# Kernel optimization log

Hardware: AMD Instinct MI355X
Metric: run time of the kernel (lower is better)

## Reference

```python
import jax, jax.numpy as jnp
import numpy as np
from jax import lax

KSIZE = 3
STRIDE = 1
RATE = 2
SCALE = 10.0
GROUPS = 4
RATES = (1, 2, 4, 8)
ESCAPE_NAN = 1e-4


def extract_patches(x, kernel, stride):
    # x: [N,C,H,W]; ZeroPad2d(1) when kernel != 1, then sliding windows.
    pad = 0 if kernel == 1 else 1
    x = jnp.pad(x, ((0, 0), (0, 0), (pad, pad), (pad, pad)))
    N, C, H, W = x.shape
    oh = (H - kernel) // stride + 1
    ow = (W - kernel) // stride + 1
    r = jnp.arange(oh)[:, None] * stride + jnp.arange(kernel)[None, :]  # [oh,k]
    c = jnp.arange(ow)[:, None] * stride + jnp.arange(kernel)[None, :]  # [ow,k]
    p = x[:, :, r[:, :, None, None], c[None, None, :, :]]  # [N,C,oh,k,ow,k]
    p = p.transpose(0, 2, 4, 1, 3, 5)  # [N,oh,ow,C,k,k] (matches torch unfold order)
    return p.reshape(N, oh * ow, C, kernel, kernel)


def make_mask_c(H, W):
    # Vectorized version of the O(H*W) nested python loop: 4-neighbor patch bias.
    ii, jj = jnp.meshgrid(jnp.arange(H), jnp.arange(W), indexing='ij')
    p = ii * W + jj
    mc = jnp.zeros((H * W, H, W), jnp.float32)
    mc = mc.at[p[:, 1:] - 1, ii[:, 1:], jj[:, 1:]].set(1.0)        # j>=1
    mc = mc.at[p[:, :-1] + 1, ii[:, :-1], jj[:, :-1]].set(1.0)     # j<=W-2
    mc = mc.at[p[:-1] + W, ii[:-1], jj[:-1]].set(1.0)              # i<=H-2
    mc = mc.at[p[1:] - W, ii[1:], jj[1:]].set(1.0)                 # i>=1
    return mc


def atn_conv(x1, x2, mask, mask_all, fuse_w, fuse_b):
    N, C1, H1, W1 = x1.shape
    _, C2, H2, W2 = x2.shape
    kernel = 2 * RATE
    # patch banks
    raw_w = extract_patches(x1, kernel, RATE * STRIDE)          # [N,L,C1,4,4]
    w = extract_patches(x2, KSIZE, STRIDE)                      # [N,L,C2,3,3]
    # mask interpolated to x2 size with align_corners=True == identity here
    m = extract_patches(mask, KSIZE, STRIDE)                    # [N,L,1,3,3]
    m = m.mean(axis=(2, 3, 4))                                  # [N,L]
    mm = (m == 0.0).astype(x2.dtype)                            # 1 = valid patch
    mask_c = make_mask_c(H2, W2)                                # [L,H2,W2]
    pad = 0 if KSIZE == 1 else 1
    kt = kernel - 1 - 1  # conv_transpose padding=1 -> equiv fwd pad k-1-p

    def per_batch(xi, wi, raw_wi, mi, ma):
        # xi [C2,H2,W2], wi [L,C2,3,3], raw_wi [L,C1,4,4], mi [L], ma [1,H2,W2]
        norm = jnp.sqrt(jnp.sum(wi * wi, axis=(1, 2, 3), keepdims=True))
        wi_n = wi / jnp.maximum(norm, ESCAPE_NAN)
        yi = lax.conv_general_dilated(xi[None], wi_n, (1, 1), [(pad, pad), (pad, pad)],
                                      dimension_numbers=('NCHW', 'OIHW', 'NCHW'))[0]  # [L,H2,W2]
        mi_b = mi[:, None, None]
        yi = yi * mi_b * ma
        yi = jax.nn.softmax(yi * SCALE, axis=0)
        yi = yi + yi * mask_c * 0.5
        yi = yi * mi_b * ma
        yi = jnp.maximum(yi, 1e-8)
        # conv_transpose2d(yi, raw_wi, stride=RATE, padding=1)
        w_t = jnp.flip(raw_wi, axis=(-2, -1))  # [L,C1,4,4] used as IOHW
        out = lax.conv_general_dilated(yi[None], w_t, (1, 1), [(kt, kt), (kt, kt)],
                                       lhs_dilation=(RATE, RATE),
                                       dimension_numbers=('NCHW', 'IOHW', 'NCHW'))[0]
        return out / 4.0  # [C1,H1,W1]

    y = jax.vmap(per_batch)(x2, w, raw_w, mm, mask_all)          # [N,C1,H1,W1]

    # fuse: 4 dilated conv+relu branches, concat on channels
    outs = []
    for g in range(GROUPS):
        d = RATES[g]
        o = lax.conv_general_dilated(y, fuse_w[g], (1, 1), [(d, d), (d, d)],
                                     rhs_dilation=(d, d),
                                     dimension_numbers=('NCHW', 'OIHW', 'NCHW'))
        outs.append(jax.nn.relu(o + fuse_b[g][None, :, None, None]))
    return jnp.concatenate(outs, axis=1)


def setup_inputs() -> dict:
    key = jax.random.key(0)
    k1, k2, k3, k4, k5 = jax.random.split(key, 5)
    N, C, H2, W2 = 2, 128, 48, 48
    x1 = jax.random.normal(k1, (N, C, 2 * H2, 2 * W2), jnp.float32)
    x2 = jax.random.normal(k2, (N, C, H2, W2), jnp.float32)
    mask = jnp.zeros((N, 1, H2, W2), jnp.float32).at[:, :, 12:36, 12:36].set(1.0)  # 1 = hole
    mask_all = jax.random.uniform(k3, (N, 1, H2, W2), jnp.float32)
    out_pg = 64 // GROUPS
    fuse_w = jax.random.normal(k4, (GROUPS, out_pg, C, 3, 3), jnp.float32) * 0.02
    fuse_b = jax.random.normal(k5, (GROUPS, out_pg), jnp.float32) * 0.02
    return {'x1': x1, 'x2': x2, 'mask': mask, 'mask_all': mask_all,
            'fuse_w': fuse_w, 'fuse_b': fuse_b}


def reference(x1, x2, mask, mask_all, fuse_w, fuse_b):
    return atn_conv(x1, x2, mask, mask_all, fuse_w, fuse_b)
```

## Files before the change

kernel.cpp:

```cpp
#include <hip/hip_runtime.h>
#include <math.h>

typedef unsigned short u16;
typedef unsigned int   u32;
typedef float f32x4 __attribute__((ext_vector_type(4)));
typedef short bfx8  __attribute__((ext_vector_type(8)));

#define NB   2
#define CCH  128
#define HS   48
#define LL   2304
#define KW   2048
#define HO   96
#define PIX  9216
#define VHALF ((size_t)LL * KW)

#define XTH_B 0
#define XTL_B 1179648
#define PXN_B 2359296
#define NRM_B 2377728
#define MM_B  2396160
#define WF_B  2414592
#define WT_B  2562048
#define S_B   11999232
#define TBD_B S_B
#define V_B   (S_B + 10616832)
#define Z_B   33232896
#define YT_B  54466560

__device__ __forceinline__ u16 f2bf(float f) {
    u32 u = __float_as_uint(f);
    u32 r = (u + 0x7fffu + ((u >> 16) & 1u)) >> 16;
    return (u16)r;
}
__device__ __forceinline__ float bf2f(u16 h) {
    return __uint_as_float(((u32)h) << 16);
}
__device__ __forceinline__ void gll16(const void* g, void* l) {
    __builtin_amdgcn_global_load_lds((const __attribute__((address_space(1))) void*)g,
                                     (__attribute__((address_space(3))) void*)l, 16, 0, 0);
}

__global__ __launch_bounds__(256) void xprep_k(const float* __restrict__ x2,
                                               u16* __restrict__ Xh, u16* __restrict__ Xl,
                                               float* __restrict__ pxn) {
    __shared__ float lt[32][130];
    int n = blockIdx.z;
    int pix0 = blockIdx.x * 32;
    int tid = threadIdx.x;
    #pragma unroll
    for (int i = tid; i < 32 * 128; i += 256) {
        int c = i >> 5, p = i & 31;
        lt[p][c] = x2[((size_t)(n * CCH + c)) * LL + pix0 + p];
    }
    __syncthreads();
    #pragma unroll
    for (int i = tid; i < 32 * 128; i += 256) {
        int p = i >> 7, c = i & 127;
        float v = lt[p][c];
        u16 h = f2bf(v);
        size_t o = (size_t)(n * LL + pix0 + p) * CCH + c;
        Xh[o] = h;
        Xl[o] = f2bf(v - bf2f(h));
    }
    if (tid < 32) {
        float s = 0.0f;
        for (int c = 0; c < CCH; c++) { float t = lt[tid][c]; s += t * t; }
        pxn[n * LL + pix0 + tid] = s;
    }
}

__global__ __launch_bounds__(256) void boxnorm_k(const float* __restrict__ pxn,
                                                 const float* __restrict__ mask,
                                                 float* __restrict__ rnorm,
                                                 float* __restrict__ mmb) {
    int n = blockIdx.z;
    int p = blockIdx.x * 256 + threadIdx.x;
    int i = p / HS, j = p - (p / HS) * HS;
    float s = 0.0f, msum = 0.0f;
    for (int di = -1; di <= 1; di++)
        for (int dj = -1; dj <= 1; dj++) {
            int ii = i + di, jj = j + dj;
            if (ii >= 0 && ii < HS && jj >= 0 && jj < HS) {
                s += pxn[n * LL + ii * HS + jj];
                msum += mask[(n * HS + ii) * HS + jj];
            }
        }
    rnorm[n * LL + p] = 1.0f / fmaxf(sqrtf(s), 1e-4f);
    mmb[n * LL + p] = (msum == 0.0f) ? 1.0f : 0.0f;
}

__global__ __launch_bounds__(256) void sgemm_k(const u16* __restrict__ Xh, const u16* __restrict__ Xl,
                                               float* __restrict__ S) {
    __shared__ __align__(16) u16 Ah[4096], Al[4096], Bh[4096], Bl[4096];
    int tid = threadIdx.x, w = tid >> 6, lane = tid & 63;
    int m0 = blockIdx.x * 128, n0 = blockIdx.y * 128;
    int srow = lane & 15, sk = (lane >> 4) * 8;
    size_t a1 = (size_t)(m0 + w * 16 + srow) * CCH + sk;
    size_t a2 = a1 + (size_t)64 * CCH;
    size_t b1 = (size_t)(n0 + w * 16 + srow) * CCH + sk;
    size_t b2 = b1 + (size_t)64 * CCH;
    int wm = (w >> 1) * 64, wn = (w & 1) * 64;
    int ga = (w >> 1) * 4, gb = (w & 1) * 4;
    f32x4 acc[4][4];
    #pragma unroll
    for (int i = 0; i < 4; i++)
        #pragma unroll
        for (int j = 0; j < 4; j++) acc[i][j] = (f32x4)0.0f;

    for (int k0 = 0; k0 < CCH; k0 += 32) {
        if (k0) __syncthreads();
        gll16(Xh + a1 + k0, Ah + w * 512);
        gll16(Xh + a2 + k0, Ah + (w + 4) * 512);
        gll16(Xl + a1 + k0, Al + w * 512);
        gll16(Xl + a2 + k0, Al + (w + 4) * 512);
        gll16(Xh + b1 + k0, Bh + w * 512);
        gll16(Xh + b2 + k0, Bh + (w + 4) * 512);
        gll16(Xl + b1 + k0, Bl + w * 512);
        gll16(Xl + b2 + k0, Bl + (w + 4) * 512);
        __syncthreads();
        bfx8 ah[4], al[4], bh[4], bl[4];
        #pragma unroll
        for (int i = 0; i < 4; i++) {
            ah[i] = *(const bfx8*)&Ah[(ga + i) * 512 + lane * 8];
            al[i] = *(const bfx8*)&Al[(ga + i) * 512 + lane * 8];
        }
        #pragma unroll
        for (int j = 0; j < 4; j++) {
            bh[j] = *(const bfx8*)&Bh[(gb + j) * 512 + lane * 8];
            bl[j] = *(const bfx8*)&Bl[(gb + j) * 512 + lane * 8];
        }
        #pragma unroll
        for (int i = 0; i < 4; i++)
            #pragma unroll
            for (int j = 0; j < 4; j++) {
                acc[i][j] = __builtin_amdgcn_mfma_f32_16x16x32_bf16(ah[i], bh[j], acc[i][j], 0, 0, 0);
                acc[i][j] = __builtin_amdgcn_mfma_f32_16x16x32_bf16(ah[i], bl[j], acc[i][j], 0, 0, 0);
                acc[i][j] = __builtin_amdgcn_mfma_f32_16x16x32_bf16(al[i], bh[j], acc[i][j], 0, 0, 0);
            }
    }
    #pragma unroll
    for (int j = 0; j < 4; j++) {
        int col = n0 + wn + j * 16 + (lane & 15);
        #pragma unroll
        for (int i = 0; i < 4; i++) {
            int rbase = m0 + wm + i * 16 + (lane >> 4) * 4;
            #pragma unroll
            for (int r = 0; r < 4; r++)
                S[(size_t)(rbase + r) * LL + col] = acc[i][j][r];
        }
    }
}

__global__ __launch_bounds__(256) void zsum_k(const float* __restrict__ S,
                                              float* __restrict__ Z) {
    __shared__ float lt[3][48][49];
    int pi = blockIdx.x, li = blockIdx.y;
    int tid = threadIdx.x;
    #pragma unroll
    for (int di = 0; di < 3; di++) {
        int a = pi + di - 1, b = li + di - 1;
        bool valid = (a >= 0) && (a < HS) && (b >= 0) && (b < HS);
        const float* base = S + ((size_t)a * HS) * LL + b * HS;
        #pragma unroll
        for (int k = 0; k < 9; k++) {
            int idx = tid + k * 256;
            int r = idx / HS, c = idx - r * HS;
            lt[di][r][c] = valid ? base[(size_t)r * LL + c] : 0.0f;
        }
    }
    __syncthreads();
    #pragma unroll
    for (int k = 0; k < 9; k++) {
        int idx = tid + k * 256;
        int pj = idx / HS, lj = idx - pj * HS;
        float acc = 0.0f;
        #pragma unroll
        for (int dj = -1; dj <= 1; dj++) {
            int rr = pj + dj, cc = lj + dj;
            if (rr >= 0 && rr < HS && cc >= 0 && cc < HS)
                acc += lt[0][rr][cc] + lt[1][rr][cc] + lt[2][rr][cc];
        }
        Z[((size_t)pi * HS + pj) * LL + li * HS + lj] = acc;
    }
}

__global__ __launch_bounds__(256) void softmax_k(const float* __restrict__ Z,
                                                 u16* __restrict__ Tb,
                                                 const float* __restrict__ rnorm,
                                                 const float* __restrict__ mmb,
                                                 const float* __restrict__ mask_all, int n) {
    int p = blockIdx.x, tid = threadIdx.x;
    __shared__ float red[8];
    const float* row = Z + (size_t)p * LL;
    u16* orow = Tb + (size_t)p * LL;
    float ma = mask_all[n * LL + p];
    float v[9], m9[9];
    float mx = -3.0e38f;
    #pragma unroll
    for (int e = 0; e < 9; e++) {
        int l = tid + e * 256;
        float m_ = mmb[n * LL + l];
        m9[e] = m_;
        float s = row[l] * rnorm[n * LL + l] * m_ * ma * 10.0f;
        v[e] = s;
        mx = fmaxf(mx, s);
    }
    #pragma unroll
    for (int o = 32; o; o >>= 1) mx = fmaxf(mx, __shfl_down(mx, o));
    int wid = tid >> 6, lane = tid & 63;
    if (lane == 0) red[wid] = mx;
    __syncthreads();
    mx = fmaxf(fmaxf(red[0], red[1]), fmaxf(red[2], red[3]));
    float sum = 0.0f;
    #pragma unroll
    for (int e = 0; e < 9; e++) { v[e] = __expf(v[e] - mx); sum += v[e]; }
    #pragma unroll
    for (int o = 32; o; o >>= 1) sum += __shfl_down(sum, o);
    if (lane == 0) red[4 + wid] = sum;
    __syncthreads();
    float inv = 1.0f / (red[4] + red[5] + red[6] + red[7]);
    int pi = p / HS, pj = p - (p / HS) * HS;
    #pragma unroll
    for (int e = 0; e < 9; e++) {
        int l = tid + e * 256;
        int li = l / HS, lj = l - li * HS;
        bool nb = (li == pi && (lj == pj - 1 || lj == pj + 1)) ||
                  (lj == pj && (li == pi - 1 || li == pi + 1));
        float z = v[e] * inv * (nb ? 1.5f : 1.0f) * m9[e] * ma;
        orow[l] = f2bf(fmaxf(z, 1e-8f));
    }
}

__global__ __launch_bounds__(256) void build_W_k(const float* __restrict__ x1,
                                                 u16* __restrict__ Wt, int n) {
    int idx = blockIdx.x * 256 + threadIdx.x;
    int l = idx % LL, f = idx / LL;
    int c = f & 127, tap = f >> 7;
    int ky = tap >> 2, kx = tap & 3;
    int li = l / HS, lj = l - (l / HS) * HS;
    int yy = 2 * li - 1 + ky, xx = 2 * lj - 1 + kx;
    float v = 0.0f;
    if (yy >= 0 && yy < HO && xx >= 0 && xx < HO)
        v = x1[((n * CCH + c) * HO + yy) * HO + xx];
    Wt[idx] = f2bf(v);
}

__global__ __launch_bounds__(256) void gemm2_k(const u16* __restrict__ Tb, const u16* __restrict__ Wt,
                                               u16* __restrict__ V) {
    __shared__ __align__(16) u16 As[8192], Bs[8192];
    int tid = threadIdx.x, w = tid >> 6, lane = tid & 63;
    int m0 = blockIdx.x * 128, n0 = blockIdx.y * 128;
    int koff = blockIdx.z * 768;
    int srow = lane & 15, sk = (lane >> 4) * 8;
    size_t a1 = (size_t)(m0 + w * 16 + srow) * LL + koff + sk;
    size_t a2 = a1 + (size_t)64 * LL;
    size_t b1 = (size_t)(n0 + w * 16 + srow) * LL + koff + sk;
    size_t b2 = b1 + (size_t)64 * LL;
    int wm = (w >> 1) * 64, wn = (w & 1) * 64;
    int ga = (w >> 1) * 4, gb = (w & 1) * 4;
    f32x4 acc[4][4];
    #pragma unroll
    for (int i = 0; i < 4; i++)
        #pragma unroll
        for (int j = 0; j < 4; j++) acc[i][j] = (f32x4)0.0f;

    for (int k0 = 0; k0 < 768; k0 += 64) {
        if (k0) __syncthreads();
        gll16(Tb + a1 + k0,      As + w * 1024);
        gll16(Tb + a1 + k0 + 32, As + w * 1024 + 512);
        gll16(Tb + a2 + k0,      As + (w + 4) * 1024);
        gll16(Tb + a2 + k0 + 32, As + (w + 4) * 1024 + 512);
        gll16(Wt + b1 + k0,      Bs + w * 1024);
        gll16(Wt + b1 + k0 + 32, Bs + w * 1024 + 512);
        gll16(Wt + b2 + k0,      Bs + (w + 4) * 1024);
        gll16(Wt + b2 + k0 + 32, Bs + (w + 4) * 1024 + 512);
        __syncthreads();
        #pragma unroll
        for (int kk = 0; kk < 2; kk++) {
            bfx8 af[4], bf[4];
            #pragma unroll
            for (int i = 0; i < 4; i++) af[i] = *(const bfx8*)&As[(ga + i) * 1024 + kk * 512 + lane * 8];
            #pragma unroll
            for (int j = 0; j < 4; j++) bf[j] = *(const bfx8*)&Bs[(gb + j) * 1024 + kk * 512 + lane * 8];
            #pragma unroll
            for (int i = 0; i < 4; i++)
                #pragma unroll
                for (int j = 0; j < 4; j++)
                    acc[i][j] = __builtin_amdgcn_mfma_f32_16x16x32_bf16(af[i], bf[j], acc[i][j], 0, 0, 0);
        }
    }
    u16* Vb = V + (size_t)blockIdx.z * VHALF;
    #pragma unroll
    for (int j = 0; j < 4; j++) {
        int f = n0 + wn + j * 16 + (lane & 15);
        #pragma unroll
        for (int i = 0; i < 4; i++) {
            int rbase = m0 + wm + i * 16 + (lane >> 4) * 4;
            #pragma unroll
            for (int r = 0; r < 4; r++)
                Vb[(size_t)(rbase + r) * KW + f] = f2bf(0.25f * acc[i][j][r]);
        }
    }
}

__global__ __launch_bounds__(256) void gather_k(const u16* __restrict__ V,
                                                u16* __restrict__ yT, int n) {
    int idx = blockIdx.x * 256 + threadIdx.x;
    int c = idx & 127, pix = idx >> 7;
    int yy = pix / HO, xx = pix - yy * HO;
    int ky0 = (yy + 1) & 1, kx0 = (xx + 1) & 1;
    float s = 0.0f;
    #pragma unroll
    for (int a = 0; a < 2; a++) {
        int ky = ky0 + a * 2;
        int py = yy + 1 - ky;
        if (py < 0 || py >= HO) continue;
        int pi = py >> 1;
        #pragma unroll
        for (int b = 0; b < 2; b++) {
            int kx = kx0 + b * 2;
            int px = xx + 1 - kx;
            if (px < 0 || px >= HO) continue;
            int pj = px >> 1;
            size_t off = (size_t)(pi * HS + pj) * KW + (ky * 4 + kx) * 128 + c;
            s += bf2f(V[off]) + bf2f(V[VHALF + off]) + bf2f(V[2 * VHALF + off]);
        }
    }
    yT[(size_t)(n * PIX + pix) * CCH + c] = f2bf(s);
}

__global__ __launch_bounds__(256) void wprep_k(const float* __restrict__ fw,
                                               u16* __restrict__ Wf) {
    int idx = blockIdx.x * 256 + threadIdx.x;
    int c = idx & 127;
    int tap = (idx >> 7) % 9;
    int go = idx / (128 * 9);
    Wf[idx] = f2bf(fw[((size_t)go * 128 + c) * 9 + tap]);
}

__global__ __launch_bounds__(256) void fuse_mfma_k(const u16* __restrict__ yT,
                                                   const u16* __restrict__ Wf,
                                                   const float* __restrict__ fb,
                                                   float* __restrict__ out) {
    int n = blockIdx.z, g = blockIdx.y;
    const int d = 1 << g;
    int tid = threadIdx.x, wv = tid >> 6, lane = tid & 63;
    int pix0 = blockIdx.x * 64 + wv * 16;
    int h = pix0 / HO, w0 = pix0 - h * HO;
    int m = lane & 15, q = lane >> 4;
    int oc = m;
    const u16* brow = Wf + ((size_t)(g * 16 + oc) * 9) * CCH + q * 8;
    f32x4 acc = (f32x4)0.0f;

    #pragma unroll
    for (int tap = 0; tap < 9; tap++) {
        int dy = (tap / 3 - 1) * d, dx = (tap % 3 - 1) * d;
        int hh = h + dy;
        int ww = w0 + m + dx;
        bool v = (hh >= 0) & (hh < HO) & (ww >= 0) & (ww < HO);
        const u16* arow = yT + ((size_t)(n * PIX + hh * HO + ww)) * CCH + q * 8;
        const u16* bt = brow + tap * CCH;
        #pragma unroll
        for (int c0 = 0; c0 < CCH; c0 += 32) {
            bfx8 af = (bfx8)0;
            if (v) af = *(const bfx8*)(arow + c0);
            bfx8 bf = *(const bfx8*)(bt + c0);
            acc = __builtin_amdgcn_mfma_f32_16x16x32_bf16(af, bf, acc, 0, 0, 0);
        }
    }
    float bias = fb[g * 16 + oc];
    f32x4 o;
    #pragma unroll
    for (int r = 0; r < 4; r++) o[r] = fmaxf(acc[r] + bias, 0.0f);
    size_t oi = ((size_t)(n * 64 + g * 16 + oc)) * PIX + pix0 + q * 4;
    *(f32x4*)&out[oi] = o;
}

extern "C" void kernel_launch(void* const* d_in, const int* in_sizes, int n_in,
                              void* d_out, int out_size, void* d_ws, size_t ws_size,
                              hipStream_t stream) {
    const float* x1       = (const float*)d_in[0];
    const float* x2       = (const float*)d_in[1];
    const float* mask     = (const float*)d_in[2];
    const float* mask_all = (const float*)d_in[3];
    const float* fw       = (const float*)d_in[4];
    const float* fb       = (const float*)d_in[5];
    float* out = (float*)d_out;
    char* wsb  = (char*)d_ws;

    u16*   Xh    = (u16*)(wsb + XTH_B);
    u16*   Xl    = (u16*)(wsb + XTL_B);
    float* pxn   = (float*)(wsb + PXN_B);
    float* rnorm = (float*)(wsb + NRM_B);
    float* mmb   = (float*)(wsb + MM_B);
    u16*   Wf    = (u16*)(wsb + WF_B);
    u16*   Wt    = (u16*)(wsb + WT_B);
    float* S     = (float*)(wsb + S_B);
    u16*   Tb    = (u16*)(wsb + TBD_B);
    u16*   V     = (u16*)(wsb + V_B);
    float* Z     = (float*)(wsb + Z_B);
    u16*   yT    = (u16*)(wsb + YT_B);

    wprep_k<<<(64 * 9 * 128) / 256, 256, 0, stream>>>(fw, Wf);
    xprep_k<<<dim3(LL / 32, 1, NB), 256, 0, stream>>>(x2, Xh, Xl, pxn);
    boxnorm_k<<<dim3(LL / 256, 1, NB), 256, 0, stream>>>(pxn, mask, rnorm, mmb);

    for (int n = 0; n < NB; n++) {
        sgemm_k<<<dim3(18, 18), 256, 0, stream>>>(Xh + (size_t)n * LL * CCH,
                                                  Xl + (size_t)n * LL * CCH, S);
        zsum_k<<<dim3(HS, HS), 256, 0, stream>>>(S, Z);
        softmax_k<<<LL, 256, 0, stream>>>(Z, Tb, rnorm, mmb, mask_all, n);
        build_W_k<<<(KW * LL) / 256, 256, 0, stream>>>(x1, Wt, n);
        gemm2_k<<<dim3(18, 16, 3), 256, 0, stream>>>(Tb, Wt, V);
        gather_k<<<(PIX * 128) / 256, 256, 0, stream>>>(V, yT, n);
    }
    fuse_mfma_k<<<dim3(PIX / 64, 4, NB), 256, 0, stream>>>(yT, Wf, fb, out);
}
```

Before: 352.3 us.

## Exploit Gram symmetry and compact masked patches to shrink GEMM K dimension

The patch-similarity GEMM and the 3x3 box-sum kernel now compute only upper-triangular tiles and mirror them, which roughly halves that work. A new scan kernel builds a compaction map of valid (unmasked) patches, so softmax writes its output in compacted order and build_W gathers only valid patches. The second GEMM's K split then runs over the compacted, padded length, skipping columns whose softmax weight was clamped to 1e-8. This drops the tiny 1e-8 contributions from masked patches, which slightly changes the numerics. It also adds a scan launch and scattered transposed stores.

```diff
diff --git a/kernel.cpp b/kernel.cpp
--- a/kernel.cpp
+++ b/kernel.cpp
@@ -27,6 +27,9 @@
 #define V_B   (S_B + 10616832)
 #define Z_B   33232896
 #define YT_B  54466560
+#define CMAP_B 59185152
+#define LIDX_B (CMAP_B + 18432)
+#define MET_B  (LIDX_B + 18432)
 
 __device__ __forceinline__ u16 f2bf(float f) {
     u32 u = __float_as_uint(f);
@@ -90,11 +93,54 @@
     mmb[n * LL + p] = (msum == 0.0f) ? 1.0f : 0.0f;
 }
 
+__global__ __launch_bounds__(256) void scan_k(const float* __restrict__ mmb,
+                                              int* __restrict__ cmap,
+                                              int* __restrict__ lidx,
+                                              int* __restrict__ meta) {
+    int n = blockIdx.x;
+    int tid = threadIdx.x, lane = tid & 63, wid = tid >> 6;
+    __shared__ int wtot[4];
+    int base = tid * 9;
+    int flags[9], cnt = 0;
+    #pragma unroll
+    for (int e = 0; e < 9; e++) {
+        flags[e] = (mmb[n * LL + base + e] != 0.0f) ? 1 : 0;
+        cnt += flags[e];
+    }
+    int inc = cnt;
+    #pragma unroll
+    for (int o = 1; o < 64; o <<= 1) {
+        int v = __shfl_up(inc, o);
+        if (lane >= o) inc += v;
+    }
+    if (lane == 63) wtot[wid] = inc;
+    __syncthreads();
+    int woff = 0;
+    for (int wv = 0; wv < wid; wv++) woff += wtot[wv];
+    int k = woff + inc - cnt;
+    #pragma unroll
+    for (int e = 0; e < 9; e++) {
+        int l = base + e;
+        if (flags[e]) { cmap[n * LL + l] = k; lidx[n * LL + k] = l; k++; }
+        else cmap[n * LL + l] = -1;
+    }
+    if (tid == 255) {
+        int Knz = woff + inc;
+        int KA = ((Knz + 191) / 192) * 64;
+        if (KA < 64) KA = 64;
+        meta[n * 2] = Knz;
+        meta[n * 2 + 1] = KA;
+    }
+}
+
 __global__ __launch_bounds__(256) void sgemm_k(const u16* __restrict__ Xh, const u16* __restrict__ Xl,
                                                float* __restrict__ S) {
     __shared__ __align__(16) u16 Ah[4096], Al[4096], Bh[4096], Bl[4096];
     int tid = threadIdx.x, w = tid >> 6, lane = tid & 63;
-    int m0 = blockIdx.x * 128, n0 = blockIdx.y * 128;
+    int t = blockIdx.x, bi = 0;
+    while (t >= 18 - bi) { t -= 18 - bi; bi++; }
+    int bj = bi + t;
+    int m0 = bi * 128, n0 = bj * 128;
     int srow = lane & 15, sk = (lane >> 4) * 8;
     size_t a1 = (size_t)(m0 + w * 16 + srow) * CCH + sk;
     size_t a2 = a1 + (size_t)64 * CCH;
@@ -148,6 +194,8 @@
             #pragma unroll
             for (int r = 0; r < 4; r++)
                 S[(size_t)(rbase + r) * LL + col] = acc[i][j][r];
+            if (bi != bj)
+                *(f32x4*)&S[(size_t)col * LL + rbase] = acc[i][j];
         }
     }
 }
@@ -155,7 +203,9 @@
 __global__ __launch_bounds__(256) void zsum_k(const float* __restrict__ S,
                                               float* __restrict__ Z) {
     __shared__ float lt[3][48][49];
-    int pi = blockIdx.x, li = blockIdx.y;
+    int t = blockIdx.x, pi = 0;
+    while (t >= HS - pi) { t -= HS - pi; pi++; }
+    int li = pi + t;
     int tid = threadIdx.x;
     #pragma unroll
     for (int di = 0; di < 3; di++) {
@@ -183,17 +233,34 @@
         }
         Z[((size_t)pi * HS + pj) * LL + li * HS + lj] = acc;
     }
+    if (pi != li) {
+        #pragma unroll
+        for (int k = 0; k < 9; k++) {
+            int idx = tid + k * 256;
+            int lj = idx / HS, pj = idx - lj * HS;
+            float acc = 0.0f;
+            #pragma unroll
+            for (int dj = -1; dj <= 1; dj++) {
+                int rr = pj + dj, cc = lj + dj;
+                if (rr >= 0 && rr < HS && cc >= 0 && cc < HS)
+                    acc += lt[0][rr][cc] + lt[1][rr][cc] + lt[2][rr][cc];
+            }
+            Z[((size_t)li * HS + lj) * LL + pi * HS + pj] = acc;
+        }
+    }
 }
 
 __global__ __launch_bounds__(256) void softmax_k(const float* __restrict__ Z,
-                                                 u16* __restrict__ Tb,
+                                                 u16* __restrict__ Tbc,
                                                  const float* __restrict__ rnorm,
                                                  const float* __restrict__ mmb,
-                                                 const float* __restrict__ mask_all, int n) {
+                                                 const float* __restrict__ mask_all,
+                                                 const int* __restrict__ cmap,
+                                                 const int* __restrict__ meta, int n) {
     int p = blockIdx.x, tid = threadIdx.x;
     __shared__ float red[8];
     const float* row = Z + (size_t)p * LL;
-    u16* orow = Tb + (size_t)p * LL;
+    u16* orow = Tbc + (size_t)p * LL;
     float ma = mask_all[n * LL + p];
     float v[9], m9[9];
     float mx = -3.0e38f;
@@ -224,34 +291,49 @@
     #pragma unroll
     for (int e = 0; e < 9; e++) {
         int l = tid + e * 256;
-        int li = l / HS, lj = l - li * HS;
-        bool nb = (li == pi && (lj == pj - 1 || lj == pj + 1)) ||
-                  (lj == pj && (li == pi - 1 || li == pi + 1));
-        float z = v[e] * inv * (nb ? 1.5f : 1.0f) * m9[e] * ma;
-        orow[l] = f2bf(fmaxf(z, 1e-8f));
-    }
+        int cm = cmap[n * LL + l];
+        if (cm >= 0) {
+            int li = l / HS, lj = l - li * HS;
+            bool nb = (li == pi && (lj == pj - 1 || lj == pj + 1)) ||
+                      (lj == pj && (li == pi - 1 || li == pi + 1));
+            float z = v[e] * inv * (nb ? 1.5f : 1.0f) * m9[e] * ma;
+            orow[cm] = f2bf(fmaxf(z, 1e-8f));
+        }
+    }
+    int Knz = meta[n * 2], KA3 = 3 * meta[n * 2 + 1];
+    for (int k = Knz + tid; k < KA3; k += 256) orow[k] = 0;
 }
 
 __global__ __launch_bounds__(256) void build_W_k(const float* __restrict__ x1,
-                                                 u16* __restrict__ Wt, int n) {
+                                                 u16* __restrict__ Wtc,
+                                                 const int* __restrict__ lidx,
+                                                 const int* __restrict__ meta, int n) {
     int idx = blockIdx.x * 256 + threadIdx.x;
-    int l = idx % LL, f = idx / LL;
-    int c = f & 127, tap = f >> 7;
-    int ky = tap >> 2, kx = tap & 3;
-    int li = l / HS, lj = l - (l / HS) * HS;
-    int yy = 2 * li - 1 + ky, xx = 2 * lj - 1 + kx;
-    float v = 0.0f;
-    if (yy >= 0 && yy < HO && xx >= 0 && xx < HO)
-        v = x1[((n * CCH + c) * HO + yy) * HO + xx];
-    Wt[idx] = f2bf(v);
-}
-
-__global__ __launch_bounds__(256) void gemm2_k(const u16* __restrict__ Tb, const u16* __restrict__ Wt,
-                                               u16* __restrict__ V) {
+    int k = idx % LL, f = idx / LL;
+    int Knz = meta[n * 2];
+    u16 out = 0;
+    if (k < Knz) {
+        int l = lidx[n * LL + k];
+        int c = f & 127, tap = f >> 7;
+        int ky = tap >> 2, kx = tap & 3;
+        int li = l / HS, lj = l - (l / HS) * HS;
+        int yy = 2 * li - 1 + ky, xx = 2 * lj - 1 + kx;
+        float v = 0.0f;
+        if (yy >= 0 && yy < HO && xx >= 0 && xx < HO)
+            v = x1[((n * CCH + c) * HO + yy) * HO + xx];
+        out = f2bf(v);
+    }
+    Wtc[idx] = out;
+}
+
+__global__ __launch_bounds__(256) void gemm2_k(const u16* __restrict__ Tbc, const u16* __restrict__ Wtc,
+                                               u16* __restrict__ V,
+                                               const int* __restrict__ meta, int n) {
     __shared__ __align__(16) u16 As[8192], Bs[8192];
     int tid = threadIdx.x, w = tid >> 6, lane = tid & 63;
     int m0 = blockIdx.x * 128, n0 = blockIdx.y * 128;
-    int koff = blockIdx.z * 768;
+    int KA = meta[n * 2 + 1];
+    int koff = blockIdx.z * KA;
     int srow = lane & 15, sk = (lane >> 4) * 8;
     size_t a1 = (size_t)(m0 + w * 16 + srow) * LL + koff + sk;
     size_t a2 = a1 + (size_t)64 * LL;
@@ -265,16 +347,16 @@
         #pragma unroll
         for (int j = 0; j < 4; j++) acc[i][j] = (f32x4)0.0f;
 
-    for (int k0 = 0; k0 < 768; k0 += 64) {
+    for (int k0 = 0; k0 < KA; k0 += 64) {
         if (k0) __syncthreads();
-        gll16(Tb + a1 + k0,      As + w * 1024);
-        gll16(Tb + a1 + k0 + 32, As + w * 1024 + 512);
-        gll16(Tb + a2 + k0,      As + (w + 4) * 1024);
-        gll16(Tb + a2 + k0 + 32, As + (w + 4) * 1024 + 512);
-        gll16(Wt + b1 + k0,      Bs + w * 1024);
-        gll16(Wt + b1 + k0 + 32, Bs + w * 1024 + 512);
-        gll16(Wt + b2 + k0,      Bs + (w + 4) * 1024);
-        gll16(Wt + b2 + k0 + 32, Bs + (w + 4) * 1024 + 512);
+        gll16(Tbc + a1 + k0,      As + w * 1024);
+        gll16(Tbc + a1 + k0 + 32, As + w * 1024 + 512);
+        gll16(Tbc + a2 + k0,      As + (w + 4) * 1024);
+        gll16(Tbc + a2 + k0 + 32, As + (w + 4) * 1024 + 512);
+        gll16(Wtc + b1 + k0,      Bs + w * 1024);
+        gll16(Wtc + b1 + k0 + 32, Bs + w * 1024 + 512);
+        gll16(Wtc + b2 + k0,      Bs + (w + 4) * 1024);
+        gll16(Wtc + b2 + k0 + 32, Bs + (w + 4) * 1024 + 512);
         __syncthreads();
         #pragma unroll
         for (int kk = 0; kk < 2; kk++) {
@@ -395,24 +477,28 @@
     float* rnorm = (float*)(wsb + NRM_B);
     float* mmb   = (float*)(wsb + MM_B);
     u16*   Wf    = (u16*)(wsb + WF_B);
-    u16*   Wt    = (u16*)(wsb + WT_B);
+    u16*   Wtc   = (u16*)(wsb + WT_B);
     float* S     = (float*)(wsb + S_B);
-    u16*   Tb    = (u16*)(wsb + TBD_B);
+    u16*   Tbc   = (u16*)(wsb + TBD_B);
     u16*   V     = (u16*)(wsb + V_B);
     float* Z     = (float*)(wsb + Z_B);
     u16*   yT    = (u16*)(wsb + YT_B);
+    int*   cmap  = (int*)(wsb + CMAP_B);
+    int*   lidx  = (int*)(wsb + LIDX_B);
+    int*   meta  = (int*)(wsb + MET_B);
 
     wprep_k<<<(64 * 9 * 128) / 256, 256, 0, stream>>>(fw, Wf);
     xprep_k<<<dim3(LL / 32, 1, NB), 256, 0, stream>>>(x2, Xh, Xl, pxn);
     boxnorm_k<<<dim3(LL / 256, 1, NB), 256, 0, stream>>>(pxn, mask, rnorm, mmb);
+    scan_k<<<NB, 256, 0, stream>>>(mmb, cmap, lidx, meta);
 
     for (int n = 0; n < NB; n++) {
-        sgemm_k<<<dim3(18, 18), 256, 0, stream>>>(Xh + (size_t)n * LL * CCH,
-                                                  Xl + (size_t)n * LL * CCH, S);
-        zsum_k<<<dim3(HS, HS), 256, 0, stream>>>(S, Z);
-        softmax_k<<<LL, 256, 0, stream>>>(Z, Tb, rnorm, mmb, mask_all, n);
-        build_W_k<<<(KW * LL) / 256, 256, 0, stream>>>(x1, Wt, n);
-        gemm2_k<<<dim3(18, 16, 3), 256, 0, stream>>>(Tb, Wt, V);
+        sgemm_k<<<171, 256, 0, stream>>>(Xh + (size_t)n * LL * CCH,
+                                         Xl + (size_t)n * LL * CCH, S);
+        zsum_k<<<HS * (HS + 1) / 2, 256, 0, stream>>>(S, Z);
+        softmax_k<<<LL, 256, 0, stream>>>(Z, Tbc, rnorm, mmb, mask_all, cmap, meta, n);
+        build_W_k<<<(KW * LL) / 256, 256, 0, stream>>>(x1, Wtc, lidx, meta, n);
+        gemm2_k<<<dim3(18, 16, 3), 256, 0, stream>>>(Tbc, Wtc, V, meta, n);
         gather_k<<<(PIX * 128) / 256, 256, 0, stream>>>(V, yT, n);
     }
     fuse_mfma_k<<<dim3(PIX / 64, 4, NB), 256, 0, stream>>>(yT, Wf, fb, out);
```

Measured after the change: 325.6 us. -7.6%, faster.
